# Kernel tuning notes

Hardware: AMD Instinct MI355X
Metric: run time of the kernel (lower is better)

## Reference

```python
import jax, jax.numpy as jnp
import numpy as np

B=64; HW=14; E=2048; L=30; V=10000; EMB=512; AML=768; ADL=500
D=512+ADL   # decoder_dim + article_downlen = 1012
A=512+ADL   # attention_dim + article_downlen = 1012

def setup_inputs() -> dict:
    key = jax.random.key(0)
    ks = jax.random.split(key, 20)
    s = 0.02
    lin = lambda k, i, o: (jax.random.normal(k, (i, o), jnp.float32) * s)
    inp = {}
    inp['encoder_out'] = jax.random.normal(ks[0], (B, HW, HW, E), jnp.float32)
    inp['encoded_captions'] = jax.random.randint(ks[1], (B, L), 0, V)
    cl = jax.random.randint(ks[2], (B, 1), 2, L + 1)
    inp['caption_lengths'] = cl.at[0, 0].set(L)  # ensure max decode length == L-1
    inp['encoded_articles'] = jax.random.normal(ks[3], (B, 1, AML), jnp.float32)
    inp['article_lengths'] = jax.random.randint(ks[4], (B, 1), 1, AML)
    inp['blank_context'] = 0
    inp['E_emb'] = jax.random.uniform(ks[5], (V, EMB), jnp.float32, -0.1, 0.1)
    inp['W_par'] = lin(ks[6], AML, ADL); inp['b_par'] = jnp.zeros(ADL, jnp.float32)
    inp['W_enc'] = lin(ks[7], E, A);     inp['b_enc'] = jnp.zeros(A, jnp.float32)
    inp['W_dec'] = lin(ks[8], D, A);     inp['b_dec'] = jnp.zeros(A, jnp.float32)
    inp['W_full'] = lin(ks[9], A, 1);    inp['b_full'] = jnp.zeros(1, jnp.float32)
    inp['W_h'] = lin(ks[10], E + ADL, D); inp['b_h'] = jnp.zeros(D, jnp.float32)
    inp['W_c'] = lin(ks[11], E + ADL, D); inp['b_c'] = jnp.zeros(D, jnp.float32)
    inp['W_fb'] = lin(ks[12], D, E);      inp['b_fb'] = jnp.zeros(E, jnp.float32)
    inp['W_ih'] = lin(ks[13], EMB + E, 4 * D); inp['b_ih'] = jnp.zeros(4 * D, jnp.float32)
    inp['W_hh'] = lin(ks[14], D, 4 * D);       inp['b_hh'] = jnp.zeros(4 * D, jnp.float32)
    inp['W_fc'] = jax.random.uniform(ks[15], (D, V), jnp.float32, -0.1, 0.1)
    inp['b_fc'] = jnp.zeros(V, jnp.float32)
    return inp

def reference(encoder_out, encoded_captions, caption_lengths, encoded_articles,
              article_lengths, blank_context, E_emb, W_par, b_par, W_enc, b_enc,
              W_dec, b_dec, W_full, b_full, W_h, b_h, W_c, b_c, W_fb, b_fb,
              W_ih, b_ih, W_hh, b_hh, W_fc, b_fc):
    Bv = encoder_out.shape[0]
    enc = encoder_out.reshape(Bv, -1, encoder_out.shape[-1])  # (B, P, E)
    lens = caption_lengths[:, 0]
    sort_ind = jnp.argsort(-lens)
    lens = lens[sort_ind]
    enc = enc[sort_ind]
    caps = encoded_captions[sort_ind]
    arts = encoded_articles[sort_ind]
    emb = E_emb[caps]                                   # (B, L, EMB)
    context = (arts @ W_par + b_par)[:, 0, :]           # ParagraphEncoder -> (B, ADL)
    dec_in = jnp.concatenate([enc.mean(axis=1), context], axis=1)
    h0 = dec_in @ W_h + b_h
    c0 = dec_in @ W_c + b_c
    dlens = lens - 1
    att1 = enc @ W_enc + b_enc                          # loop-invariant, (B, P, A)
    T = emb.shape[1] - 1

    def step(carry, t):
        h, c = carry
        active = (dlens > t)[:, None]                   # prefix mask (sorted desc)
        att2 = h @ W_dec + b_dec
        scores = (jax.nn.relu(att1 + att2[:, None, :]) @ W_full)[..., 0] + b_full[0]
        alpha = jax.nn.softmax(scores, axis=1)          # (B, P)
        awe = jnp.einsum('bp,bpe->be', alpha, enc)
        awe = jax.nn.sigmoid(h @ W_fb + b_fb) * awe     # gated attention encoding
        x = jnp.concatenate([emb[:, t, :], awe], axis=1)
        gates = x @ W_ih + b_ih + h @ W_hh + b_hh       # torch LSTMCell, gate order i,f,g,o
        i, f, g, o = jnp.split(gates, 4, axis=1)
        c_new = jax.nn.sigmoid(f) * c + jax.nn.sigmoid(i) * jnp.tanh(g)
        h_new = jax.nn.sigmoid(o) * jnp.tanh(c_new)
        preds = jnp.where(active, h_new @ W_fc + b_fc, 0.0)
        alpha_m = jnp.where(active, alpha, 0.0)
        h = jnp.where(active, h_new, h)
        c = jnp.where(active, c_new, c)
        return (h, c), (preds, alpha_m)

    _, (preds, alphas) = jax.lax.scan(step, (h0, c0), jnp.arange(T))
    predictions = jnp.transpose(preds, (1, 0, 2))       # (B, T, V)
    alphas = jnp.transpose(alphas, (1, 0, 2))           # (B, T, P)
    return (predictions, caps, dlens, alphas, sort_ind)
```

## Files before the change

### kernel.cpp

```cpp
#include <hip/hip_runtime.h>
#include <math.h>

#define B_   64
#define P_   196
#define E_   2048
#define L_   30
#define T_   29
#define V_   10000
#define EMB_ 512
#define AML_ 768
#define ADL_ 500
#define D_   1012
#define A_   1012
#define G4_  4048
#define XK_  2560

typedef unsigned short u16;
typedef __attribute__((ext_vector_type(8))) short bf16x8;
typedef __attribute__((ext_vector_type(4))) float f32x4;

__device__ __forceinline__ float sigf(float x) { return 1.f / (1.f + __expf(-x)); }
__device__ __forceinline__ float tanhf_fast(float x) { return 1.f - 2.f / (__expf(2.f * x) + 1.f); }
__device__ __forceinline__ u16 f2bf(float f) {
    unsigned u = __float_as_uint(f);
    return (u16)((u + 0x7FFFu + ((u >> 16) & 1u)) >> 16);
}
__device__ __forceinline__ float bf2f(u16 v) { return __uint_as_float(((unsigned)v) << 16); }

__global__ void k_setup(const int* __restrict__ clen, const int* __restrict__ caps,
                        float* __restrict__ out_caps, float* __restrict__ out_dlens,
                        float* __restrict__ out_sind,
                        int* __restrict__ sort_ind, int* __restrict__ dlens_i,
                        int* __restrict__ nact, int* __restrict__ caps_s)
{
    __shared__ int lens[B_];
    int t = threadIdx.x;
    if (t < B_) lens[t] = clen[t];
    __syncthreads();
    if (t < B_) {
        int my = lens[t];
        int rank = 0;
        for (int j = 0; j < B_; ++j) {
            int lj = lens[j];
            if (lj > my || (lj == my && j < t)) rank++;
        }
        sort_ind[rank] = t;
    }
    __syncthreads();
    if (t < B_) {
        int orig = sort_ind[t];
        int dl = lens[orig] - 1;
        dlens_i[t] = dl;
        out_dlens[t] = (float)dl;
        out_sind[t] = (float)orig;
        for (int j = 0; j < L_; ++j) {
            int cv = caps[orig * L_ + j];
            caps_s[t * L_ + j] = cv;
            out_caps[t * L_ + j] = (float)cv;
        }
    }
    __syncthreads();
    if (t < T_) {
        int cnt = 0;
        for (int j = 0; j < B_; ++j) cnt += (dlens_i[j] > t) ? 1 : 0;
        nact[t] = cnt;
    }
}

__global__ void k_zero(float4* __restrict__ p, long n4)
{
    long i = (long)blockIdx.x * 256 + threadIdx.x;
    if (i < n4) p[i] = make_float4(0.f, 0.f, 0.f, 0.f);
}

__global__ void k_cvt_enc(const float* __restrict__ enc, const int* __restrict__ sort_ind,
                          u16* __restrict__ A_bf)
{
    int row = blockIdx.y;
    int b = row / 196, p = row - b * 196;
    int e4 = (blockIdx.x * 256 + threadIdx.x) * 4;
    const float* src = enc + ((long)sort_ind[b] * 196 + p) * E_ + e4;
    float4 v = *(const float4*)src;
    unsigned lo = (unsigned)f2bf(v.x) | ((unsigned)f2bf(v.y) << 16);
    unsigned hi = (unsigned)f2bf(v.z) | ((unsigned)f2bf(v.w) << 16);
    uint2 pk; pk.x = lo; pk.y = hi;
    *(uint2*)(A_bf + (long)row * E_ + e4) = pk;
}

__global__ void k_transpose(const float* __restrict__ src, u16* __restrict__ dst,
                            int K, int N, int Kp, int Np)
{
    __shared__ float tile[32][33];
    int n0 = blockIdx.x * 32, k0 = blockIdx.y * 32;
    int tx = threadIdx.x, ty = threadIdx.y;
    for (int r = ty; r < 32; r += 8) {
        int k = k0 + r, n = n0 + tx;
        tile[r][tx] = (k < K && n < N) ? src[(long)k * N + n] : 0.f;
    }
    __syncthreads();
    for (int r = ty; r < 32; r += 8) {
        int n = n0 + r, k = k0 + tx;
        if (n < Np && k < Kp) dst[(long)n * Kp + k] = f2bf(tile[tx][r]);
    }
}

__global__ void k_encmean(const float* __restrict__ enc, const int* __restrict__ sort_ind,
                          u16* __restrict__ dec_in)
{
    int b = blockIdx.y;
    int e = blockIdx.x * 256 + threadIdx.x;
    int orig = sort_ind[b];
    const float* src = enc + (long)orig * P_ * E_ + e;
    float s = 0.f;
    for (int p = 0; p < P_; ++p) s += src[(long)p * E_];
    dec_in[(long)b * XK_ + e] = f2bf(s * (1.f / 196.f));
}

__global__ void k_ctx(const float* __restrict__ arts, const float* __restrict__ W_par,
                      const float* __restrict__ b_par, const int* __restrict__ sort_ind,
                      u16* __restrict__ dec_in)
{
    int b = blockIdx.y;
    int k = blockIdx.x * 256 + threadIdx.x;
    if (k >= 512) return;
    float s = 0.f;
    if (k < ADL_) {
        int orig = sort_ind[b];
        const float* ar = arts + (long)orig * AML_;
        s = b_par[k];
        for (int m = 0; m < AML_; ++m) s = fmaf(ar[m], W_par[m * ADL_ + k], s);
    }
    dec_in[(long)b * XK_ + E_ + k] = f2bf(s);
}

__global__ void k_emb_all(const float* __restrict__ E_emb, const int* __restrict__ caps_s,
                          u16* __restrict__ emb_all)
{
    int t = blockIdx.x;
    int b = blockIdx.y;
    int tok = caps_s[b * L_ + t];
    for (int k = threadIdx.x; k < EMB_; k += 256)
        emb_all[((long)t * B_ + b) * EMB_ + k] = f2bf(E_emb[(long)tok * EMB_ + k]);
}

__global__ void __launch_bounds__(256) k_att1_mfma(
    const u16* __restrict__ A, const u16* __restrict__ W,
    const float* __restrict__ bias, u16* __restrict__ Yb)
{
    int w = threadIdx.x >> 6, lane = threadIdx.x & 63;
    int lr = lane & 15, lk = (lane >> 4) * 8;
    int n0 = blockIdx.x * 256 + w * 64;
    int r0 = blockIdx.y * 64;
    f32x4 acc[4][4];
#pragma unroll
    for (int i = 0; i < 4; ++i)
#pragma unroll
        for (int j = 0; j < 4; ++j) acc[i][j] = (f32x4){0.f, 0.f, 0.f, 0.f};
    const u16* ap = A + (long)(r0 + lr) * E_ + lk;
    const u16* wp = W + (long)(n0 + lr) * E_ + lk;
    for (int k = 0; k < E_; k += 32) {
        bf16x8 af[4], bf[4];
#pragma unroll
        for (int mt = 0; mt < 4; ++mt) af[mt] = *(const bf16x8*)(ap + (long)mt * 16 * E_ + k);
#pragma unroll
        for (int nt = 0; nt < 4; ++nt) bf[nt] = *(const bf16x8*)(wp + (long)nt * 16 * E_ + k);
#pragma unroll
        for (int mt = 0; mt < 4; ++mt)
#pragma unroll
            for (int nt = 0; nt < 4; ++nt)
                acc[mt][nt] = __builtin_amdgcn_mfma_f32_16x16x32_bf16(af[mt], bf[nt], acc[mt][nt], 0, 0, 0);
    }
#pragma unroll
    for (int mt = 0; mt < 4; ++mt) {
#pragma unroll
        for (int nt = 0; nt < 4; ++nt) {
            int n = n0 + nt * 16 + lr;
            float bv = (n < A_) ? bias[n] : 0.f;
#pragma unroll
            for (int j = 0; j < 4; ++j) {
                int row = r0 + mt * 16 + (lane >> 4) * 4 + j;
                u16 outv = (n < A_) ? f2bf(acc[mt][nt][j] + bv) : (u16)0;
                Yb[(long)row * 1024 + n] = outv;
            }
        }
    }
}

template <int ACT, int OUT, int PADZ>
__global__ void __launch_bounds__(256) k_skinny(
    const u16* __restrict__ A1, const u16* __restrict__ W1, int K1,
    const float* __restrict__ bias1, void* __restrict__ Yv,
    long ldY, long offY, int Nmax,
    const int* __restrict__ nact, int t)
{
    int Bact = (t >= 0) ? nact[t] : B_;
    if (Bact <= 0) return;
    int mmax = (Bact + 15) >> 4;
    int w = threadIdx.x >> 6, lane = threadIdx.x & 63;
    int lr = lane & 15, lk = (lane >> 4) * 8;
    int n0 = blockIdx.x * 64 + w * 16;
    f32x4 acc[4];
#pragma unroll
    for (int m = 0; m < 4; ++m) acc[m] = (f32x4){0.f, 0.f, 0.f, 0.f};

    int n = n0 + lr;
    int nc = n < Nmax ? n : Nmax - 1;
    const u16* a1p = A1 + (long)lr * K1 + lk;
    const u16* w1p = W1 + (long)nc * K1 + lk;
    for (int k = 0; k < K1; k += 32) {
        bf16x8 bw = *(const bf16x8*)(w1p + k);
#pragma unroll
        for (int m = 0; m < 4; ++m)
            if (m < mmax) {
                bf16x8 aw = *(const bf16x8*)(a1p + (long)m * 16 * K1 + k);
                acc[m] = __builtin_amdgcn_mfma_f32_16x16x32_bf16(aw, bw, acc[m], 0, 0, 0);
            }
    }
    float bv = (n < Nmax) ? bias1[n] : 0.f;
#pragma unroll
    for (int m = 0; m < 4; ++m) {
        if (m < mmax) {
#pragma unroll
            for (int j = 0; j < 4; ++j) {
                int b = m * 16 + (lane >> 4) * 4 + j;
                if (b < Bact) {
                    float v = acc[m][j] + bv;
                    if (ACT == 1) v = sigf(v);
                    if (n < Nmax) {
                        if (OUT == 1) ((u16*)Yv)[(long)b * ldY + offY + n] = f2bf(v);
                        else          ((float*)Yv)[(long)b * ldY + offY + n] = v;
                    } else if (PADZ) {
                        if (OUT == 1) ((u16*)Yv)[(long)b * ldY + offY + n] = 0;
                        else          ((float*)Yv)[(long)b * ldY + offY + n] = 0.f;
                    }
                }
            }
        }
    }
}

__global__ void __launch_bounds__(256) k_att2fb(
    const u16* __restrict__ h_bf, const u16* __restrict__ WT_dec,
    const u16* __restrict__ WT_fb, const float* __restrict__ b_dec,
    const float* __restrict__ b_fb, float* __restrict__ att2p,
    float* __restrict__ fbp, const int* __restrict__ nact, int t)
{
    int Bact = nact[t];
    if (Bact <= 0) return;
    int mmax = (Bact + 15) >> 4;
    int kh = blockIdx.x >= 48;
    int nb = blockIdx.x - (kh ? 48 : 0);
    int isfb = nb >= 16;
    const u16* W = isfb ? WT_fb : WT_dec;
    const float* bias = isfb ? b_fb : b_dec;
    int Nmax = isfb ? E_ : A_;
    int nb2 = isfb ? nb - 16 : nb;
    long ldY = isfb ? (long)E_ : 1024L;
    float* Y = (isfb ? fbp : att2p) + (long)kh * B_ * ldY;

    int w = threadIdx.x >> 6, lane = threadIdx.x & 63;
    int lr = lane & 15, lk = (lane >> 4) * 8;
    int n = nb2 * 64 + w * 16 + lr;
    int nc = n < Nmax ? n : Nmax - 1;
    int k0 = kh * 512;
    f32x4 acc[4];
#pragma unroll
    for (int m = 0; m < 4; ++m) acc[m] = (f32x4){0.f, 0.f, 0.f, 0.f};
    const u16* ap = h_bf + (long)lr * 1024 + k0 + lk;
    const u16* wp = W + (long)nc * 1024 + k0 + lk;
    for (int k = 0; k < 512; k += 32) {
        bf16x8 bw = *(const bf16x8*)(wp + k);
#pragma unroll
        for (int m = 0; m < 4; ++m)
            if (m < mmax) {
                bf16x8 aw = *(const bf16x8*)(ap + (long)m * 16 * 1024 + k);
                acc[m] = __builtin_amdgcn_mfma_f32_16x16x32_bf16(aw, bw, acc[m], 0, 0, 0);
            }
    }
    if (n >= Nmax) return;
    float bv = (kh == 0) ? bias[n] : 0.f;
#pragma unroll
    for (int m = 0; m < 4; ++m) {
        if (m < mmax) {
#pragma unroll
            for (int j = 0; j < 4; ++j) {
                int b = m * 16 + (lane >> 4) * 4 + j;
                if (b < Bact) Y[(long)b * ldY + n] = acc[m][j] + bv;
            }
        }
    }
}

__global__ void k_scores(const u16* __restrict__ att1, const float* __restrict__ att2p,
                         const float* __restrict__ W_full, const float* __restrict__ b_full,
                         float* __restrict__ scores, const int* __restrict__ nact, int t)
{
    int b = blockIdx.y;
    if (b >= nact[t]) return;
    int wv = threadIdx.x >> 6;
    int lane = threadIdx.x & 63;
    int p = blockIdx.x * 4 + wv;
    const u16* a1 = att1 + ((long)b * P_ + p) * 1024;
    const float* a20 = att2p + (long)b * 1024;
    const float* a21 = att2p + (long)B_ * 1024 + (long)b * 1024;
    float acc = 0.f;
    for (int j2 = lane; j2 < 506; j2 += 64) {
        unsigned pk = *(const unsigned*)(a1 + 2 * j2);
        float2 p0 = *(const float2*)(a20 + 2 * j2);
        float2 p1 = *(const float2*)(a21 + 2 * j2);
        float2 wv2 = *(const float2*)(W_full + 2 * j2);
        float v0 = bf2f((u16)(pk & 0xFFFF)) + p0.x + p1.x;
        float v1 = bf2f((u16)(pk >> 16)) + p0.y + p1.y;
        v0 = v0 > 0.f ? v0 : 0.f;
        v1 = v1 > 0.f ? v1 : 0.f;
        acc = fmaf(v0, wv2.x, acc);
        acc = fmaf(v1, wv2.y, acc);
    }
    for (int m = 32; m >= 1; m >>= 1) acc += __shfl_xor(acc, m);
    if (lane == 0) scores[b * P_ + p] = acc + b_full[0];
}

__global__ void __launch_bounds__(256) k_awe_x(
    const u16* __restrict__ A_bf, const float* __restrict__ scores,
    const float* __restrict__ fbp, u16* __restrict__ awe_buf,
    float* __restrict__ alphas_out, const int* __restrict__ nact, int t)
{
    int b = blockIdx.y;
    if (b >= nact[t]) return;
    int tid = threadIdx.x;
    int w = tid >> 6, lane = tid & 63;
    __shared__ float al[P_];
    __shared__ float red[4];
    float v = (tid < P_) ? scores[b * P_ + tid] : -1e30f;
    float m = v;
    for (int s = 32; s >= 1; s >>= 1) m = fmaxf(m, __shfl_xor(m, s));
    if (lane == 0) red[w] = m;
    __syncthreads();
    m = fmaxf(fmaxf(red[0], red[1]), fmaxf(red[2], red[3]));
    float e = (tid < P_) ? __expf(v - m) : 0.f;
    float s_ = e;
    for (int s = 32; s >= 1; s >>= 1) s_ += __shfl_xor(s_, s);
    __syncthreads();
    if (lane == 0) red[w] = s_;
    __syncthreads();
    s_ = red[0] + red[1] + red[2] + red[3];
    if (tid < P_) al[tid] = e / s_;
    __syncthreads();

    if (blockIdx.x < 8) {
        int e0 = blockIdx.x * 256 + tid;
        const u16* src = A_bf + (long)b * P_ * E_ + e0;
        float s0 = 0.f, s1 = 0.f, s2 = 0.f, s3 = 0.f;
        for (int p = 0; p < P_; p += 4) {
            s0 = fmaf(al[p],     bf2f(src[(long)p * E_]), s0);
            s1 = fmaf(al[p + 1], bf2f(src[(long)(p + 1) * E_]), s1);
            s2 = fmaf(al[p + 2], bf2f(src[(long)(p + 2) * E_]), s2);
            s3 = fmaf(al[p + 3], bf2f(src[(long)(p + 3) * E_]), s3);
        }
        float g = sigf(fbp[(long)b * E_ + e0] + fbp[(long)(B_ + b) * E_ + e0]);
        awe_buf[(long)b * E_ + e0] = f2bf((s0 + s1 + s2 + s3) * g);
    } else {
        if (tid < P_) alphas_out[((long)b * T_ + t) * P_ + tid] = al[tid];
    }
}

__global__ void __launch_bounds__(256) k_gates(
    const u16* __restrict__ emb_t, const u16* __restrict__ awe,
    const u16* __restrict__ h_old, const u16* __restrict__ WT_ih,
    const u16* __restrict__ WT_hh, float* __restrict__ gpart,
    const int* __restrict__ nact, int t)
{
    int Bact = nact[t];
    if (Bact <= 0) return;
    int mmax = (Bact + 15) >> 4;
    int q = threadIdx.x >> 6;
    int lane = threadIdx.x & 63;
    int lr = lane & 15, lk = (lane >> 4) * 8;
    int kh = blockIdx.y;
    int n = blockIdx.x * 16 + lr;
    int nc = n < D_ ? n : D_ - 1;
    f32x4 acc[4];
#pragma unroll
    for (int m = 0; m < 4; ++m) acc[m] = (f32x4){0.f, 0.f, 0.f, 0.f};
    const u16* wih = WT_ih + ((long)q * D_ + nc) * XK_;
    const u16* whh = WT_hh + ((long)q * D_ + nc) * 1024;

    if (kh == 0) {
        const u16* ap = emb_t + (long)lr * EMB_ + lk;
        for (int k = 0; k < EMB_; k += 32) {
            bf16x8 bw = *(const bf16x8*)(wih + k);
#pragma unroll
            for (int m = 0; m < 4; ++m)
                if (m < mmax) {
                    bf16x8 aw = *(const bf16x8*)(ap + (long)m * 16 * EMB_ + k);
                    acc[m] = __builtin_amdgcn_mfma_f32_16x16x32_bf16(aw, bw, acc[m], 0, 0, 0);
                }
        }
        const u16* ap2 = awe + (long)lr * E_ + lk;
        const u16* w2 = wih + EMB_;
        for (int k = 0; k < 1280; k += 32) {
            bf16x8 bw = *(const bf16x8*)(w2 + k);
#pragma unroll
            for (int m = 0; m < 4; ++m)
                if (m < mmax) {
                    bf16x8 aw = *(const bf16x8*)(ap2 + (long)m * 16 * E_ + k);
                    acc[m] = __builtin_amdgcn_mfma_f32_16x16x32_bf16(aw, bw, acc[m], 0, 0, 0);
                }
        }
    } else {
        const u16* ap2 = awe + (long)lr * E_ + 1280 + lk;
        const u16* w2 = wih + 1792;
        for (int k = 0; k < 768; k += 32) {
            bf16x8 bw = *(const bf16x8*)(w2 + k);
#pragma unroll
            for (int m = 0; m < 4; ++m)
                if (m < mmax) {
                    bf16x8 aw = *(const bf16x8*)(ap2 + (long)m * 16 * E_ + k);
                    acc[m] = __builtin_amdgcn_mfma_f32_16x16x32_bf16(aw, bw, acc[m], 0, 0, 0);
                }
        }
        const u16* ap3 = h_old + (long)lr * 1024 + lk;
        for (int k = 0; k < 1024; k += 32) {
            bf16x8 bw = *(const bf16x8*)(whh + k);
#pragma unroll
            for (int m = 0; m < 4; ++m)
                if (m < mmax) {
                    bf16x8 aw = *(const bf16x8*)(ap3 + (long)m * 16 * 1024 + k);
                    acc[m] = __builtin_amdgcn_mfma_f32_16x16x32_bf16(aw, bw, acc[m], 0, 0, 0);
                }
        }
    }
#pragma unroll
    for (int m = 0; m < 4; ++m) {
        if (m < mmax) {
#pragma unroll
            for (int j = 0; j < 4; ++j) {
                int bb = m * 16 + (lane >> 4) * 4 + j;
                if (bb < Bact)
                    gpart[((long)kh * B_ + bb) * 4096 + q * 1024 + n] = acc[m][j];
            }
        }
    }
}

__global__ void k_lstm_red(const float* __restrict__ gpart, const float* __restrict__ b_ih,
                           const float* __restrict__ b_hh, float* __restrict__ cbuf,
                           u16* __restrict__ h_new, const int* __restrict__ nact, int t)
{
    int b = blockIdx.y;
    if (b >= nact[t]) return;
    int n = blockIdx.x * 256 + threadIdx.x;
    if (n >= D_) return;
    const float* g0 = gpart + (long)b * 4096;
    const float* g1 = gpart + (long)(B_ + b) * 4096;
    float gi = g0[n]        + g1[n]        + b_ih[n]          + b_hh[n];
    float gf = g0[1024 + n] + g1[1024 + n] + b_ih[D_ + n]     + b_hh[D_ + n];
    float gg = g0[2048 + n] + g1[2048 + n] + b_ih[2 * D_ + n] + b_hh[2 * D_ + n];
    float go = g0[3072 + n] + g1[3072 + n] + b_ih[3 * D_ + n] + b_hh[3 * D_ + n];
    float c = cbuf[(long)b * 1024 + n];
    float cn = sigf(gf) * c + sigf(gi) * tanhf_fast(gg);
    float hn = sigf(go) * tanhf_fast(cn);
    cbuf[(long)b * 1024 + n] = cn;
    h_new[(long)b * 1024 + n] = f2bf(hn);
}

__global__ void __launch_bounds__(256) k_fc_all(
    const u16* __restrict__ h_all, const u16* __restrict__ W,
    const float* __restrict__ bias, float* __restrict__ out_preds,
    const int* __restrict__ nact)
{
    int tslot = blockIdx.y;
    int Bact = nact[tslot];
    if (Bact <= 0) return;
    int mmax = (Bact + 15) >> 4;
    int w = threadIdx.x >> 6, lane = threadIdx.x & 63;
    int lr = lane & 15, lk = (lane >> 4) * 8;
    int n0 = blockIdx.x * 256 + w * 64;
    f32x4 acc[4][4];
#pragma unroll
    for (int i = 0; i < 4; ++i)
#pragma unroll
        for (int j = 0; j < 4; ++j) acc[i][j] = (f32x4){0.f, 0.f, 0.f, 0.f};
    const u16* ap = h_all + ((long)(tslot + 1) * B_ + lr) * 1024 + lk;
    int ncl[4];
#pragma unroll
    for (int nt = 0; nt < 4; ++nt) {
        int n = n0 + nt * 16 + lr;
        ncl[nt] = n < V_ ? n : V_ - 1;
    }
    for (int k = 0; k < 1024; k += 32) {
        bf16x8 af[4], bf[4];
#pragma unroll
        for (int mt = 0; mt < 4; ++mt)
            if (mt < mmax) af[mt] = *(const bf16x8*)(ap + (long)mt * 16 * 1024 + k);
#pragma unroll
        for (int nt = 0; nt < 4; ++nt) bf[nt] = *(const bf16x8*)(W + (long)ncl[nt] * 1024 + lk + k);
#pragma unroll
        for (int mt = 0; mt < 4; ++mt)
            if (mt < mmax)
#pragma unroll
                for (int nt = 0; nt < 4; ++nt)
                    acc[mt][nt] = __builtin_amdgcn_mfma_f32_16x16x32_bf16(af[mt], bf[nt], acc[mt][nt], 0, 0, 0);
    }
#pragma unroll
    for (int nt = 0; nt < 4; ++nt) {
        int n = n0 + nt * 16 + lr;
        if (n >= V_) continue;
        float bv = bias[n];
#pragma unroll
        for (int mt = 0; mt < 4; ++mt) {
            if (mt < mmax) {
#pragma unroll
                for (int j = 0; j < 4; ++j) {
                    int b = mt * 16 + (lane >> 4) * 4 + j;
                    if (b < Bact)
                        out_preds[(long)b * T_ * V_ + (long)tslot * V_ + n] = acc[mt][nt][j] + bv;
                }
            }
        }
    }
}

extern "C" void kernel_launch(void* const* d_in, const int* in_sizes, int n_in,
                              void* d_out, int out_size, void* d_ws, size_t ws_size,
                              hipStream_t stream)
{
    const float* enc    = (const float*)d_in[0];
    const int*   caps   = (const int*)d_in[1];
    const int*   clen   = (const int*)d_in[2];
    const float* arts   = (const float*)d_in[3];
    const float* E_emb  = (const float*)d_in[6];
    const float* W_par  = (const float*)d_in[7];
    const float* b_par  = (const float*)d_in[8];
    const float* W_enc  = (const float*)d_in[9];
    const float* b_enc  = (const float*)d_in[10];
    const float* W_dec  = (const float*)d_in[11];
    const float* b_dec  = (const float*)d_in[12];
    const float* W_full = (const float*)d_in[13];
    const float* b_full = (const float*)d_in[14];
    const float* W_h    = (const float*)d_in[15];
    const float* b_h    = (const float*)d_in[16];
    const float* W_c    = (const float*)d_in[17];
    const float* b_c    = (const float*)d_in[18];
    const float* W_fb   = (const float*)d_in[19];
    const float* b_fb   = (const float*)d_in[20];
    const float* W_ih   = (const float*)d_in[21];
    const float* b_ih   = (const float*)d_in[22];
    const float* W_hh   = (const float*)d_in[23];
    const float* b_hh   = (const float*)d_in[24];
    const float* W_fc   = (const float*)d_in[25];
    const float* b_fc   = (const float*)d_in[26];

    float* out = (float*)d_out;
    float* out_preds  = out;
    float* out_caps   = out + (long)B_ * T_ * V_;
    float* out_dlens  = out_caps + B_ * L_;
    float* out_alphas = out_dlens + B_;
    float* out_sind   = out_alphas + (long)B_ * T_ * P_;

    float* ws = (float*)d_ws;
    long o = 0;
    auto alloc = [&](long n) { long r = o; o += (n + 63) & ~63L; return r; };
    long o_ints   = alloc(2176);
    long o_decin  = alloc((long)B_ * XK_ / 2);
    long o_hall   = alloc((long)(T_ + 1) * B_ * 1024 / 2);
    long o_emball = alloc((long)T_ * B_ * EMB_ / 2);
    long o_awe    = alloc((long)B_ * E_ / 2);
    long o_c      = alloc((long)B_ * 1024);
    long o_att2p  = alloc((long)2 * B_ * 1024);
    long o_fbp    = alloc((long)2 * B_ * E_);
    long o_gpart  = alloc((long)2 * B_ * 4096);
    long o_scores = alloc((long)B_ * P_);
    long o_Abf    = alloc((long)12544 * E_ / 2);
    long o_att1   = alloc((long)12544 * 1024 / 2);
    long o_wtenc  = alloc((long)1024 * 2048 / 2);
    long o_wtdec  = alloc((long)1024 * 1024 / 2);
    long o_wtfb   = alloc((long)2048 * 1024 / 2);
    long o_wtih   = alloc((long)4096 * 2560 / 2);
    long o_wthh   = alloc((long)4096 * 1024 / 2);
    long o_wtfc   = alloc((long)10048 * 1024 / 2);

    int* sort_ind = (int*)(ws + o_ints);
    int* dlens_i  = sort_ind + 64;
    int* nact     = dlens_i + 64;
    int* caps_s   = nact + 32;
    u16*   dec_in  = (u16*)(ws + o_decin);
    u16*   h_all   = (u16*)(ws + o_hall);
    u16*   emb_all = (u16*)(ws + o_emball);
    u16*   awe_buf = (u16*)(ws + o_awe);
    float* cbuf   = ws + o_c;
    float* att2p  = ws + o_att2p;
    float* fbp    = ws + o_fbp;
    float* gpart  = ws + o_gpart;
    float* scores = ws + o_scores;
    u16*   A_bf   = (u16*)(ws + o_Abf);
    u16*   att1   = (u16*)(ws + o_att1);
    u16*   WT_enc = (u16*)(ws + o_wtenc);
    u16*   WT_dec = (u16*)(ws + o_wtdec);
    u16*   WT_fb  = (u16*)(ws + o_wtfb);
    u16*   WT_ih  = (u16*)(ws + o_wtih);
    u16*   WT_hh  = (u16*)(ws + o_wthh);
    u16*   WT_fc  = (u16*)(ws + o_wtfc);
    u16*   WT_h   = att1;
    u16*   WT_c   = att1 + (long)1024 * XK_;

    long n4 = ((long)B_ * T_ * V_ + B_ * L_ + B_ + (long)B_ * T_ * P_ + B_) / 4;
    k_zero<<<dim3((unsigned)((n4 + 255) / 256)), 256, 0, stream>>>((float4*)d_out, n4);
    k_setup<<<1, 64, 0, stream>>>(clen, caps, out_caps, out_dlens, out_sind,
                                  sort_ind, dlens_i, nact, caps_s);

    k_encmean<<<dim3(8, 64), 256, 0, stream>>>(enc, sort_ind, dec_in);
    k_ctx<<<dim3(2, 64), 256, 0, stream>>>(arts, W_par, b_par, sort_ind, dec_in);
    k_emb_all<<<dim3(T_, 64), 256, 0, stream>>>(E_emb, caps_s, emb_all);

    dim3 tb(32, 8);
    k_transpose<<<dim3(1024/32, 2560/32), tb, 0, stream>>>(W_h, WT_h, 2548, 1012, 2560, 1024);
    k_transpose<<<dim3(1024/32, 2560/32), tb, 0, stream>>>(W_c, WT_c, 2548, 1012, 2560, 1024);
    k_skinny<0,1,1><<<dim3(16), 256, 0, stream>>>(dec_in, WT_h, XK_, b_h, h_all, 1024L, 0L, D_,
                                                  nact, -1);
    k_skinny<0,0,1><<<dim3(16), 256, 0, stream>>>(dec_in, WT_c, XK_, b_c, cbuf, 1024L, 0L, D_,
                                                  nact, -1);

    k_transpose<<<dim3(1024/32, 2048/32), tb, 0, stream>>>(W_enc, WT_enc, 2048, 1012, 2048, 1024);
    k_transpose<<<dim3(1024/32, 1024/32), tb, 0, stream>>>(W_dec, WT_dec, 1012, 1012, 1024, 1024);
    k_transpose<<<dim3(2048/32, 1024/32), tb, 0, stream>>>(W_fb, WT_fb, 1012, 2048, 1024, 2048);
    k_transpose<<<dim3(4096/32, 2560/32), tb, 0, stream>>>(W_ih, WT_ih, 2560, 4048, 2560, 4096);
    k_transpose<<<dim3(4096/32, 1024/32), tb, 0, stream>>>(W_hh, WT_hh, 1012, 4048, 1024, 4096);
    k_transpose<<<dim3(10048/32, 1024/32), tb, 0, stream>>>(W_fc, WT_fc, 1012, 10000, 1024, 10048);

    k_cvt_enc<<<dim3(2, 12544), 256, 0, stream>>>(enc, sort_ind, A_bf);
    k_att1_mfma<<<dim3(4, 196), 256, 0, stream>>>(A_bf, WT_enc, b_enc, att1);

    for (int t = 0; t < T_; ++t) {
        const u16* h_old = h_all + (long)t * B_ * 1024;
        u16* h_new = h_all + (long)(t + 1) * B_ * 1024;
        const u16* emb_t = emb_all + (long)t * B_ * EMB_;
        k_att2fb<<<dim3(96), 256, 0, stream>>>(h_old, WT_dec, WT_fb, b_dec, b_fb,
                                               att2p, fbp, nact, t);
        k_scores<<<dim3(49, 64), 256, 0, stream>>>(att1, att2p, W_full, b_full, scores, nact, t);
        k_awe_x<<<dim3(9, 64), 256, 0, stream>>>(A_bf, scores, fbp, awe_buf,
                                                 out_alphas, nact, t);
        k_gates<<<dim3(64, 2), 256, 0, stream>>>(emb_t, awe_buf, h_old, WT_ih, WT_hh,
                                                 gpart, nact, t);
        k_lstm_red<<<dim3(4, 64), 256, 0, stream>>>(gpart, b_ih, b_hh, cbuf, h_new, nact, t);
    }
    k_fc_all<<<dim3(40, T_), 256, 0, stream>>>(h_all, WT_fc, b_fc, out_preds, nact);
}
```

Measured before the change: 3.111 ms.

## Move h@W_hh into the h-projection kernel and fuse gates with LSTM update

Moves the h@W_hh recurrent projection out of the gates kernel into the kernel that already computes h@W_dec and h@W_fb, which now uses the full K range and applies the sigmoid gate there. This drops the K-split partial buffers and their cross-partial sums. The gates kernel now runs 512 threads, splits K internally across 8 waves, reduces through shared memory and applies the LSTM cell update in place, which removes the separate reduction kernel launch at every timestep. The att1 GEMM tile height is also halved to double its block count. In exchange, fewer and larger blocks run on the per-step critical path, and each wave does more K iterations.

```diff
diff --git a/kernel.cpp b/kernel.cpp
--- a/kernel.cpp
+++ b/kernel.cpp
@@ -150,28 +150,28 @@
     int w = threadIdx.x >> 6, lane = threadIdx.x & 63;
     int lr = lane & 15, lk = (lane >> 4) * 8;
     int n0 = blockIdx.x * 256 + w * 64;
-    int r0 = blockIdx.y * 64;
-    f32x4 acc[4][4];
-#pragma unroll
-    for (int i = 0; i < 4; ++i)
+    int r0 = blockIdx.y * 32;
+    f32x4 acc[2][4];
+#pragma unroll
+    for (int i = 0; i < 2; ++i)
 #pragma unroll
         for (int j = 0; j < 4; ++j) acc[i][j] = (f32x4){0.f, 0.f, 0.f, 0.f};
     const u16* ap = A + (long)(r0 + lr) * E_ + lk;
     const u16* wp = W + (long)(n0 + lr) * E_ + lk;
     for (int k = 0; k < E_; k += 32) {
-        bf16x8 af[4], bf[4];
-#pragma unroll
-        for (int mt = 0; mt < 4; ++mt) af[mt] = *(const bf16x8*)(ap + (long)mt * 16 * E_ + k);
+        bf16x8 af[2], bf[4];
+#pragma unroll
+        for (int mt = 0; mt < 2; ++mt) af[mt] = *(const bf16x8*)(ap + (long)mt * 16 * E_ + k);
 #pragma unroll
         for (int nt = 0; nt < 4; ++nt) bf[nt] = *(const bf16x8*)(wp + (long)nt * 16 * E_ + k);
 #pragma unroll
-        for (int mt = 0; mt < 4; ++mt)
+        for (int mt = 0; mt < 2; ++mt)
 #pragma unroll
             for (int nt = 0; nt < 4; ++nt)
                 acc[mt][nt] = __builtin_amdgcn_mfma_f32_16x16x32_bf16(af[mt], bf[nt], acc[mt][nt], 0, 0, 0);
     }
 #pragma unroll
-    for (int mt = 0; mt < 4; ++mt) {
+    for (int mt = 0; mt < 2; ++mt) {
 #pragma unroll
         for (int nt = 0; nt < 4; ++nt) {
             int n = n0 + nt * 16 + lr;
@@ -239,36 +239,46 @@
     }
 }
 
-__global__ void __launch_bounds__(256) k_att2fb(
+__global__ void __launch_bounds__(256) k_hproj(
     const u16* __restrict__ h_bf, const u16* __restrict__ WT_dec,
-    const u16* __restrict__ WT_fb, const float* __restrict__ b_dec,
-    const float* __restrict__ b_fb, float* __restrict__ att2p,
-    float* __restrict__ fbp, const int* __restrict__ nact, int t)
+    const u16* __restrict__ WT_fb, const u16* __restrict__ WT_hh,
+    const float* __restrict__ b_dec, const float* __restrict__ b_fb,
+    float* __restrict__ att2, float* __restrict__ fbuf, float* __restrict__ gh,
+    const int* __restrict__ nact, int t)
 {
     int Bact = nact[t];
     if (Bact <= 0) return;
     int mmax = (Bact + 15) >> 4;
-    int kh = blockIdx.x >= 48;
-    int nb = blockIdx.x - (kh ? 48 : 0);
-    int isfb = nb >= 16;
-    const u16* W = isfb ? WT_fb : WT_dec;
-    const float* bias = isfb ? b_fb : b_dec;
-    int Nmax = isfb ? E_ : A_;
-    int nb2 = isfb ? nb - 16 : nb;
-    long ldY = isfb ? (long)E_ : 1024L;
-    float* Y = (isfb ? fbp : att2p) + (long)kh * B_ * ldY;
-
     int w = threadIdx.x >> 6, lane = threadIdx.x & 63;
     int lr = lane & 15, lk = (lane >> 4) * 8;
-    int n = nb2 * 64 + w * 16 + lr;
-    int nc = n < Nmax ? n : Nmax - 1;
-    int k0 = kh * 512;
+
+    const u16* Wbase;
+    float* Y;
+    long ldY;
+    int nloc, wrow, mode;
+    if (blockIdx.x < 16) {
+        mode = 0;
+        nloc = blockIdx.x * 64 + w * 16 + lr;
+        wrow = nloc < A_ ? nloc : A_ - 1;
+        Wbase = WT_dec; Y = att2; ldY = 1024;
+    } else if (blockIdx.x < 48) {
+        mode = 1;
+        nloc = (blockIdx.x - 16) * 64 + w * 16 + lr;
+        wrow = nloc;
+        Wbase = WT_fb; Y = fbuf; ldY = E_;
+    } else {
+        mode = 2;
+        nloc = (blockIdx.x - 48) * 64 + w * 16 + lr;
+        int q = nloc >> 10, d = nloc & 1023;
+        wrow = q * D_ + (d < D_ ? d : D_ - 1);
+        Wbase = WT_hh; Y = gh; ldY = 4096;
+    }
     f32x4 acc[4];
 #pragma unroll
     for (int m = 0; m < 4; ++m) acc[m] = (f32x4){0.f, 0.f, 0.f, 0.f};
-    const u16* ap = h_bf + (long)lr * 1024 + k0 + lk;
-    const u16* wp = W + (long)nc * 1024 + k0 + lk;
-    for (int k = 0; k < 512; k += 32) {
+    const u16* ap = h_bf + (long)lr * 1024 + lk;
+    const u16* wp = Wbase + (long)wrow * 1024 + lk;
+    for (int k = 0; k < 1024; k += 32) {
         bf16x8 bw = *(const bf16x8*)(wp + k);
 #pragma unroll
         for (int m = 0; m < 4; ++m)
@@ -277,21 +287,26 @@
                 acc[m] = __builtin_amdgcn_mfma_f32_16x16x32_bf16(aw, bw, acc[m], 0, 0, 0);
             }
     }
-    if (n >= Nmax) return;
-    float bv = (kh == 0) ? bias[n] : 0.f;
+    float bv = 0.f;
+    if (mode == 0) bv = (nloc < A_) ? b_dec[nloc] : 0.f;
+    if (mode == 1) bv = b_fb[nloc];
 #pragma unroll
     for (int m = 0; m < 4; ++m) {
         if (m < mmax) {
 #pragma unroll
             for (int j = 0; j < 4; ++j) {
                 int b = m * 16 + (lane >> 4) * 4 + j;
-                if (b < Bact) Y[(long)b * ldY + n] = acc[m][j] + bv;
+                if (b < Bact) {
+                    float v = acc[m][j] + bv;
+                    if (mode == 1) v = sigf(v);
+                    Y[(long)b * ldY + nloc] = v;
+                }
             }
         }
     }
 }
 
-__global__ void k_scores(const u16* __restrict__ att1, const float* __restrict__ att2p,
+__global__ void k_scores(const u16* __restrict__ att1, const float* __restrict__ att2,
                          const float* __restrict__ W_full, const float* __restrict__ b_full,
                          float* __restrict__ scores, const int* __restrict__ nact, int t)
 {
@@ -301,16 +316,14 @@
     int lane = threadIdx.x & 63;
     int p = blockIdx.x * 4 + wv;
     const u16* a1 = att1 + ((long)b * P_ + p) * 1024;
-    const float* a20 = att2p + (long)b * 1024;
-    const float* a21 = att2p + (long)B_ * 1024 + (long)b * 1024;
+    const float* a2 = att2 + (long)b * 1024;
     float acc = 0.f;
     for (int j2 = lane; j2 < 506; j2 += 64) {
         unsigned pk = *(const unsigned*)(a1 + 2 * j2);
-        float2 p0 = *(const float2*)(a20 + 2 * j2);
-        float2 p1 = *(const float2*)(a21 + 2 * j2);
+        float2 p0 = *(const float2*)(a2 + 2 * j2);
         float2 wv2 = *(const float2*)(W_full + 2 * j2);
-        float v0 = bf2f((u16)(pk & 0xFFFF)) + p0.x + p1.x;
-        float v1 = bf2f((u16)(pk >> 16)) + p0.y + p1.y;
+        float v0 = bf2f((u16)(pk & 0xFFFF)) + p0.x;
+        float v1 = bf2f((u16)(pk >> 16)) + p0.y;
         v0 = v0 > 0.f ? v0 : 0.f;
         v1 = v1 > 0.f ? v1 : 0.f;
         acc = fmaf(v0, wv2.x, acc);
@@ -322,7 +335,7 @@
 
 __global__ void __launch_bounds__(256) k_awe_x(
     const u16* __restrict__ A_bf, const float* __restrict__ scores,
-    const float* __restrict__ fbp, u16* __restrict__ awe_buf,
+    const float* __restrict__ fbuf, u16* __restrict__ awe_buf,
     float* __restrict__ alphas_out, const int* __restrict__ nact, int t)
 {
     int b = blockIdx.y;
@@ -357,33 +370,33 @@
             s2 = fmaf(al[p + 2], bf2f(src[(long)(p + 2) * E_]), s2);
             s3 = fmaf(al[p + 3], bf2f(src[(long)(p + 3) * E_]), s3);
         }
-        float g = sigf(fbp[(long)b * E_ + e0] + fbp[(long)(B_ + b) * E_ + e0]);
+        float g = fbuf[(long)b * E_ + e0];
         awe_buf[(long)b * E_ + e0] = f2bf((s0 + s1 + s2 + s3) * g);
     } else {
         if (tid < P_) alphas_out[((long)b * T_ + t) * P_ + tid] = al[tid];
     }
 }
 
-__global__ void __launch_bounds__(256) k_gates(
+__global__ void __launch_bounds__(512) k_gates_lstm2(
     const u16* __restrict__ emb_t, const u16* __restrict__ awe,
-    const u16* __restrict__ h_old, const u16* __restrict__ WT_ih,
-    const u16* __restrict__ WT_hh, float* __restrict__ gpart,
+    const u16* __restrict__ WT_ih, const float* __restrict__ gh,
+    const float* __restrict__ b_ih, const float* __restrict__ b_hh,
+    float* __restrict__ cbuf, u16* __restrict__ h_new,
     const int* __restrict__ nact, int t)
 {
     int Bact = nact[t];
     if (Bact <= 0) return;
     int mmax = (Bact + 15) >> 4;
-    int q = threadIdx.x >> 6;
+    int ww = threadIdx.x >> 6;
+    int q = ww & 3, kh = ww >> 2;
     int lane = threadIdx.x & 63;
     int lr = lane & 15, lk = (lane >> 4) * 8;
-    int kh = blockIdx.y;
     int n = blockIdx.x * 16 + lr;
     int nc = n < D_ ? n : D_ - 1;
     f32x4 acc[4];
 #pragma unroll
     for (int m = 0; m < 4; ++m) acc[m] = (f32x4){0.f, 0.f, 0.f, 0.f};
     const u16* wih = WT_ih + ((long)q * D_ + nc) * XK_;
-    const u16* whh = WT_hh + ((long)q * D_ + nc) * 1024;
 
     if (kh == 0) {
         const u16* ap = emb_t + (long)lr * EMB_ + lk;
@@ -398,7 +411,7 @@
         }
         const u16* ap2 = awe + (long)lr * E_ + lk;
         const u16* w2 = wih + EMB_;
-        for (int k = 0; k < 1280; k += 32) {
+        for (int k = 0; k < 768; k += 32) {
             bf16x8 bw = *(const bf16x8*)(w2 + k);
 #pragma unroll
             for (int m = 0; m < 4; ++m)
@@ -408,9 +421,9 @@
                 }
         }
     } else {
-        const u16* ap2 = awe + (long)lr * E_ + 1280 + lk;
-        const u16* w2 = wih + 1792;
-        for (int k = 0; k < 768; k += 32) {
+        const u16* ap2 = awe + (long)lr * E_ + 768 + lk;
+        const u16* w2 = wih + EMB_ + 768;
+        for (int k = 0; k < 1280; k += 32) {
             bf16x8 bw = *(const bf16x8*)(w2 + k);
 #pragma unroll
             for (int m = 0; m < 4; ++m)
@@ -419,49 +432,40 @@
                     acc[m] = __builtin_amdgcn_mfma_f32_16x16x32_bf16(aw, bw, acc[m], 0, 0, 0);
                 }
         }
-        const u16* ap3 = h_old + (long)lr * 1024 + lk;
-        for (int k = 0; k < 1024; k += 32) {
-            bf16x8 bw = *(const bf16x8*)(whh + k);
-#pragma unroll
-            for (int m = 0; m < 4; ++m)
-                if (m < mmax) {
-                    bf16x8 aw = *(const bf16x8*)(ap3 + (long)m * 16 * 1024 + k);
-                    acc[m] = __builtin_amdgcn_mfma_f32_16x16x32_bf16(aw, bw, acc[m], 0, 0, 0);
-                }
-        }
-    }
+    }
+    __shared__ float g2[8][64][17];
 #pragma unroll
     for (int m = 0; m < 4; ++m) {
         if (m < mmax) {
 #pragma unroll
             for (int j = 0; j < 4; ++j) {
                 int bb = m * 16 + (lane >> 4) * 4 + j;
-                if (bb < Bact)
-                    gpart[((long)kh * B_ + bb) * 4096 + q * 1024 + n] = acc[m][j];
+                g2[ww][bb][lr] = acc[m][j];
             }
         }
     }
-}
-
-__global__ void k_lstm_red(const float* __restrict__ gpart, const float* __restrict__ b_ih,
-                           const float* __restrict__ b_hh, float* __restrict__ cbuf,
-                           u16* __restrict__ h_new, const int* __restrict__ nact, int t)
-{
-    int b = blockIdx.y;
-    if (b >= nact[t]) return;
-    int n = blockIdx.x * 256 + threadIdx.x;
-    if (n >= D_) return;
-    const float* g0 = gpart + (long)b * 4096;
-    const float* g1 = gpart + (long)(B_ + b) * 4096;
-    float gi = g0[n]        + g1[n]        + b_ih[n]          + b_hh[n];
-    float gf = g0[1024 + n] + g1[1024 + n] + b_ih[D_ + n]     + b_hh[D_ + n];
-    float gg = g0[2048 + n] + g1[2048 + n] + b_ih[2 * D_ + n] + b_hh[2 * D_ + n];
-    float go = g0[3072 + n] + g1[3072 + n] + b_ih[3 * D_ + n] + b_hh[3 * D_ + n];
-    float c = cbuf[(long)b * 1024 + n];
-    float cn = sigf(gf) * c + sigf(gi) * tanhf_fast(gg);
-    float hn = sigf(go) * tanhf_fast(cn);
-    cbuf[(long)b * 1024 + n] = cn;
-    h_new[(long)b * 1024 + n] = f2bf(hn);
+    __syncthreads();
+#pragma unroll
+    for (int i = 0; i < 2; ++i) {
+        int idx = threadIdx.x + i * 512;
+        int bb = idx >> 4, col = idx & 15;
+        int n2 = blockIdx.x * 16 + col;
+        if (bb >= Bact) continue;
+        if (n2 >= D_) {
+            if (n2 < 1024) h_new[(long)bb * 1024 + n2] = 0;
+            continue;
+        }
+        const float* ghb = gh + (long)bb * 4096;
+        float gi = g2[0][bb][col] + g2[4][bb][col] + ghb[n2]        + b_ih[n2]          + b_hh[n2];
+        float gf = g2[1][bb][col] + g2[5][bb][col] + ghb[1024 + n2] + b_ih[D_ + n2]     + b_hh[D_ + n2];
+        float gg = g2[2][bb][col] + g2[6][bb][col] + ghb[2048 + n2] + b_ih[2 * D_ + n2] + b_hh[2 * D_ + n2];
+        float go = g2[3][bb][col] + g2[7][bb][col] + ghb[3072 + n2] + b_ih[3 * D_ + n2] + b_hh[3 * D_ + n2];
+        float c = cbuf[(long)bb * 1024 + n2];
+        float cn = sigf(gf) * c + sigf(gi) * tanhf_fast(gg);
+        float hn = sigf(go) * tanhf_fast(cn);
+        cbuf[(long)bb * 1024 + n2] = cn;
+        h_new[(long)bb * 1024 + n2] = f2bf(hn);
+    }
 }
 
 __global__ void __launch_bounds__(256) k_fc_all(
@@ -567,9 +571,9 @@
     long o_emball = alloc((long)T_ * B_ * EMB_ / 2);
     long o_awe    = alloc((long)B_ * E_ / 2);
     long o_c      = alloc((long)B_ * 1024);
-    long o_att2p  = alloc((long)2 * B_ * 1024);
-    long o_fbp    = alloc((long)2 * B_ * E_);
-    long o_gpart  = alloc((long)2 * B_ * 4096);
+    long o_att2   = alloc((long)B_ * 1024);
+    long o_fbuf   = alloc((long)B_ * E_);
+    long o_gh     = alloc((long)B_ * 4096);
     long o_scores = alloc((long)B_ * P_);
     long o_Abf    = alloc((long)12544 * E_ / 2);
     long o_att1   = alloc((long)12544 * 1024 / 2);
@@ -589,9 +593,9 @@
     u16*   emb_all = (u16*)(ws + o_emball);
     u16*   awe_buf = (u16*)(ws + o_awe);
     float* cbuf   = ws + o_c;
-    float* att2p  = ws + o_att2p;
-    float* fbp    = ws + o_fbp;
-    float* gpart  = ws + o_gpart;
+    float* att2   = ws + o_att2;
+    float* fbuf   = ws + o_fbuf;
+    float* gh     = ws + o_gh;
     float* scores = ws + o_scores;
     u16*   A_bf   = (u16*)(ws + o_Abf);
     u16*   att1   = (u16*)(ws + o_att1);
@@ -629,20 +633,19 @@
     k_transpose<<<dim3(10048/32, 1024/32), tb, 0, stream>>>(W_fc, WT_fc, 1012, 10000, 1024, 10048);
 
     k_cvt_enc<<<dim3(2, 12544), 256, 0, stream>>>(enc, sort_ind, A_bf);
-    k_att1_mfma<<<dim3(4, 196), 256, 0, stream>>>(A_bf, WT_enc, b_enc, att1);
+    k_att1_mfma<<<dim3(4, 392), 256, 0, stream>>>(A_bf, WT_enc, b_enc, att1);
 
     for (int t = 0; t < T_; ++t) {
         const u16* h_old = h_all + (long)t * B_ * 1024;
         u16* h_new = h_all + (long)(t + 1) * B_ * 1024;
         const u16* emb_t = emb_all + (long)t * B_ * EMB_;
-        k_att2fb<<<dim3(96), 256, 0, stream>>>(h_old, WT_dec, WT_fb, b_dec, b_fb,
-                                               att2p, fbp, nact, t);
-        k_scores<<<dim3(49, 64), 256, 0, stream>>>(att1, att2p, W_full, b_full, scores, nact, t);
-        k_awe_x<<<dim3(9, 64), 256, 0, stream>>>(A_bf, scores, fbp, awe_buf,
+        k_hproj<<<dim3(112), 256, 0, stream>>>(h_old, WT_dec, WT_fb, WT_hh, b_dec, b_fb,
+                                               att2, fbuf, gh, nact, t);
+        k_scores<<<dim3(49, 64), 256, 0, stream>>>(att1, att2, W_full, b_full, scores, nact, t);
+        k_awe_x<<<dim3(9, 64), 256, 0, stream>>>(A_bf, scores, fbuf, awe_buf,
                                                  out_alphas, nact, t);
-        k_gates<<<dim3(64, 2), 256, 0, stream>>>(emb_t, awe_buf, h_old, WT_ih, WT_hh,
-                                                 gpart, nact, t);
-        k_lstm_red<<<dim3(4, 64), 256, 0, stream>>>(gpart, b_ih, b_hh, cbuf, h_new, nact, t);
+        k_gates_lstm2<<<dim3(64), 512, 0, stream>>>(emb_t, awe_buf, WT_ih, gh, b_ih, b_hh,
+                                                    cbuf, h_new, nact, t);
     }
     k_fc_all<<<dim3(40, T_), 256, 0, stream>>>(h_all, WT_fc, b_fc, out_preds, nact);
 }
```

After: 3.355 ms. 1.08x slower.
